# Performance work log

Hardware: AMD Instinct MI355X
Metric: run time of the kernel (lower is better)

The kernel has to match this reference:

```python
import jax, jax.numpy as jnp
import numpy as np

B, T, L = 64, 256, 64          # batch, time steps, num_links
H = 128                        # hidden_size
E = 524288                     # num edges
N = B * T                      # nodes seen by GCNConv
IN = L + L * L                 # 4160: concat of link features + flattened distance matrix
OUT = 12 * L                   # fc output size
NUM_LSTM = 2


def setup_inputs() -> dict:
    key = jax.random.key(0)
    ks = jax.random.split(key, 24)
    inp = {
        "x": jax.random.normal(ks[0], (B, T, L), jnp.float32),
        "distance": jax.random.uniform(ks[1], (L, L), jnp.float32),
        "edge_index": jax.random.randint(ks[2], (2, E), 0, N, jnp.int64),
    }
    # GCN layer params (PyG GCNConv: lin weight [in,out] acting as x @ W, bias after aggregation)
    dims = [IN, H, H, H]
    for i in range(3):
        s = 1.0 / np.sqrt(dims[i])
        inp[f"gcn_W{i}"] = jax.random.normal(ks[3 + 2 * i], (dims[i], H), jnp.float32) * s
        inp[f"gcn_b{i}"] = jnp.zeros((H,), jnp.float32)
    # LSTM params, torch layout: W_ih [4H, Hin], W_hh [4H, H], gate order i,f,g,o
    s = 1.0 / np.sqrt(H)
    for l in range(NUM_LSTM):
        inp[f"Wih{l}"] = jax.random.normal(ks[10 + 4 * l], (4 * H, H), jnp.float32) * s
        inp[f"Whh{l}"] = jax.random.normal(ks[11 + 4 * l], (4 * H, H), jnp.float32) * s
        inp[f"bih{l}"] = jax.random.normal(ks[12 + 4 * l], (4 * H,), jnp.float32) * s
        inp[f"bhh{l}"] = jax.random.normal(ks[13 + 4 * l], (4 * H,), jnp.float32) * s
    inp["fc_W"] = jax.random.normal(ks[20], (OUT, H), jnp.float32) * s
    inp["fc_b"] = jnp.zeros((OUT,), jnp.float32)
    return inp


def _gcn(x, W, b, src, dst):
    # GCNConv with add_self_loops=True: out = D^-1/2 (A+I) D^-1/2 (x W) + b
    h = x @ W
    deg = jnp.ones((N,), h.dtype).at[dst].add(1.0)  # in-degree + self loop
    dinv = jax.lax.rsqrt(deg)
    norm = dinv[src] * dinv[dst]                    # [E]
    agg = jnp.zeros_like(h).at[dst].add(h[src] * norm[:, None])
    agg = agg + h * (dinv * dinv)[:, None]          # self-loop term
    return agg + b


def _lstm_layer(xs, Wih, Whh, bih, bhh):
    # xs: [T, B, Hin]
    bias = bih + bhh

    def step(carry, xt):
        h, c = carry
        g = xt @ Wih.T + h @ Whh.T + bias
        i, f, gg, o = jnp.split(g, 4, axis=-1)
        c = jax.nn.sigmoid(f) * c + jax.nn.sigmoid(i) * jnp.tanh(gg)
        h = jax.nn.sigmoid(o) * jnp.tanh(c)
        return (h, c), h

    h0 = jnp.zeros((xs.shape[1], H), xs.dtype)
    _, ys = jax.lax.scan(step, (h0, h0), xs)
    return ys


def reference(x, distance, gcn_W0, gcn_b0, gcn_W1, gcn_b1, gcn_W2, gcn_b2,
              Wih0, Whh0, bih0, bhh0, Wih1, Whh1, bih1, bhh1, fc_W, fc_b,
              edge_index):
    src, dst = edge_index[0], edge_index[1]
    xf = x.reshape(N, L)
    dist_flat = jnp.broadcast_to(distance.reshape(1, L * L), (N, L * L))
    feat = jnp.concatenate([xf, dist_flat], axis=1)  # [N, IN]
    for W, b in ((gcn_W0, gcn_b0), (gcn_W1, gcn_b1), (gcn_W2, gcn_b2)):
        feat = jax.nn.relu(_gcn(feat, W, b, src, dst))
    seq = feat.reshape(B, T, H).transpose(1, 0, 2)   # [T, B, H]
    seq = _lstm_layer(seq, Wih0, Whh0, bih0, bhh0)
    seq = _lstm_layer(seq, Wih1, Whh1, bih1, bhh1)
    last = seq[-1]                                   # [B, H]
    out = last @ fc_W.T + fc_b                       # [B, OUT]
    return out.reshape(B, 12, L)
```

## Files before the change

kernel.cpp:

```cpp
#include <hip/hip_runtime.h>
#include <hip/hip_bf16.h>
#include <cstdint>
#include <cstddef>

#define NB 64
#define NT 256
#define NL 64
#define NH 128
#define NN 16384
#define NE 524288
#define NG 512
#define NOUT 768


__global__ __launch_bounds__(256) void k_transpose(const float* __restrict__ W,
                                                   float* __restrict__ Wt,
                                                   int K, int Nout) {
  int i = blockIdx.x * 256 + threadIdx.x;
  if (i < K * Nout) {
    int k = i / Nout, n = i % Nout;
    Wt[n * K + k] = W[i];
  }
}

__global__ __launch_bounds__(256) void k_dvec(const float* __restrict__ dist,
                                              const float* __restrict__ W0,
                                              float* __restrict__ dvec) {
  __shared__ float red[256];
  int j = blockIdx.x;
  int t = threadIdx.x;
  float acc = 0.f;
  for (int m = t; m < 4096; m += 256)
    acc += dist[m] * W0[(size_t)(64 + m) * 128 + j];
  red[t] = acc;
  __syncthreads();
  for (int off = 128; off > 0; off >>= 1) {
    if (t < off) red[t] += red[t + off];
    __syncthreads();
  }
  if (t == 0) dvec[j] = red[0];
}

__global__ __launch_bounds__(256) void k_count(const int* __restrict__ dst,
                                               int* __restrict__ counts) {
  int i = blockIdx.x * 256 + threadIdx.x;
  atomicAdd(&counts[dst[i]], 1);
}

__global__ __launch_bounds__(256) void k_dinv(const int* __restrict__ counts,
                                              float* __restrict__ dinv) {
  int n = blockIdx.x * 256 + threadIdx.x;
  dinv[n] = rsqrtf((float)counts[n] + 1.0f);
}

__global__ __launch_bounds__(1024) void k_scan(const int* __restrict__ counts,
                                               int* __restrict__ rowstart) {
  __shared__ int part[1024];
  int t = threadIdx.x;
  int base = t * 16;
  int local[16];
  int s = 0;
#pragma unroll
  for (int i = 0; i < 16; i++) { local[i] = s; s += counts[base + i]; }
  part[t] = s;
  __syncthreads();
  for (int off = 1; off < 1024; off <<= 1) {
    int v = (t >= off) ? part[t - off] : 0;
    __syncthreads();
    part[t] += v;
    __syncthreads();
  }
  int prefix = (t == 0) ? 0 : part[t - 1];
#pragma unroll
  for (int i = 0; i < 16; i++) rowstart[base + i] = prefix + local[i];
  if (t == 1023) rowstart[16384] = part[1023];
}

__global__ __launch_bounds__(256) void k_fill(const int* __restrict__ src,
                                              const int* __restrict__ dst,
                                              const int* __restrict__ rowstart,
                                              int* __restrict__ fill,
                                              const float* __restrict__ dinv,
                                              int* __restrict__ csr_src,
                                              float* __restrict__ csr_nrm) {
  int e = blockIdx.x * 256 + threadIdx.x;
  int sN = src[e], dN = dst[e];
  int pos = rowstart[dN] + atomicAdd(&fill[dN], 1);
  csr_src[pos] = sN;
  csr_nrm[pos] = dinv[sN] * dinv[dN];
}

template <int K, bool RELU, bool PERMC = false>
__global__ __launch_bounds__(256) void k_gemm_abt(const float* __restrict__ A,
                                                  const float* __restrict__ Bm,
                                                  const float* __restrict__ bias0,
                                                  const float* __restrict__ bias1,
                                                  float* __restrict__ C, int Nn) {
  __shared__ float As[64][K + 1];
  __shared__ float Bs[64][K + 1];
  const int tid = threadIdx.x;
  const int bm = blockIdx.x, bn = blockIdx.y;
  const int VPR = K / 4;
  for (int i = tid; i < 64 * VPR; i += 256) {
    int r = i / VPR, v = (i % VPR) * 4;
    float4 q = *(const float4*)(A + (size_t)(bm * 64 + r) * K + v);
    As[r][v] = q.x; As[r][v + 1] = q.y; As[r][v + 2] = q.z; As[r][v + 3] = q.w;
  }
  for (int i = tid; i < 64 * VPR; i += 256) {
    int r = i / VPR, v = (i % VPR) * 4;
    float4 q = *(const float4*)(Bm + (size_t)(bn * 64 + r) * K + v);
    Bs[r][v] = q.x; Bs[r][v + 1] = q.y; Bs[r][v + 2] = q.z; Bs[r][v + 3] = q.w;
  }
  __syncthreads();
  const int tr = (tid >> 4) << 2;
  const int tc = (tid & 15) << 2;
  float acc[4][4] = {};
#pragma unroll 4
  for (int k = 0; k < K; k++) {
    float a0 = As[tr + 0][k], a1 = As[tr + 1][k], a2 = As[tr + 2][k], a3 = As[tr + 3][k];
    float b0 = Bs[tc + 0][k], b1 = Bs[tc + 1][k], b2 = Bs[tc + 2][k], b3 = Bs[tc + 3][k];
    acc[0][0] += a0 * b0; acc[0][1] += a0 * b1; acc[0][2] += a0 * b2; acc[0][3] += a0 * b3;
    acc[1][0] += a1 * b0; acc[1][1] += a1 * b1; acc[1][2] += a1 * b2; acc[1][3] += a1 * b3;
    acc[2][0] += a2 * b0; acc[2][1] += a2 * b1; acc[2][2] += a2 * b2; acc[2][3] += a2 * b3;
    acc[3][0] += a3 * b0; acc[3][1] += a3 * b1; acc[3][2] += a3 * b2; acc[3][3] += a3 * b3;
  }
#pragma unroll
  for (int i2 = 0; i2 < 4; i2++) {
    int row = bm * 64 + tr + i2;
#pragma unroll
    for (int j2 = 0; j2 < 4; j2++) {
      int col = bn * 64 + tc + j2;
      float v = acc[i2][j2];
      if (bias0) v += bias0[col];
      if (bias1) v += bias1[col];
      if (RELU) v = fmaxf(v, 0.f);
      int colw = PERMC ? ((col & 127) * 4 + (col >> 7)) : col;
      C[(size_t)row * Nn + colw] = v;
    }
  }
}

__global__ __launch_bounds__(256) void k_agg(const float* __restrict__ h,
                                             const int* __restrict__ rowstart,
                                             const int* __restrict__ csr_src,
                                             const float* __restrict__ csr_nrm,
                                             const float* __restrict__ dinv,
                                             const float* __restrict__ bias,
                                             float* __restrict__ out) {
  int node = blockIdx.x * 4 + (threadIdx.x >> 6);
  int lane = threadIdx.x & 63;
  int s = rowstart[node], e = rowstart[node + 1];
  float a0 = 0.f, a1 = 0.f;
  for (int p = s; p < e; p++) {
    int src = csr_src[p];
    float w = csr_nrm[p];
    a0 += h[(size_t)src * 128 + lane] * w;
    a1 += h[(size_t)src * 128 + 64 + lane] * w;
  }
  float di = dinv[node];
  float sw = di * di;
  a0 += h[(size_t)node * 128 + lane] * sw + bias[lane];
  a1 += h[(size_t)node * 128 + 64 + lane] * sw + bias[64 + lane];
  out[(size_t)node * 128 + lane] = fmaxf(a0, 0.f);
  out[(size_t)node * 128 + 64 + lane] = fmaxf(a1, 0.f);
}


template <int CTRL>
__device__ __forceinline__ float dppadd(float x) {
  int r = __builtin_amdgcn_update_dpp(0, __float_as_int(x), CTRL, 0xF, 0xF, true);
  return x + __int_as_float(r);
}

__device__ __forceinline__ float sigf(float x) {
  return 1.f / (1.f + __expf(-x));
}
__device__ __forceinline__ float tanhf_fast(float x) {
  return 1.f - 2.f / (__expf(2.f * x) + 1.f);
}

template <bool LAST_ONLY>
__global__ __launch_bounds__(512, 2) void k_lstm2(const float* __restrict__ pre,
                                                  const float* __restrict__ Whh,
                                                  float* __restrict__ yout) {
  __shared__ float hbuf[2][128];
  const int tid = threadIdx.x;
  const int b = blockIdx.x;
  const int c4 = tid & 3;
  const int u = tid >> 2;

  int hidx[8];
#pragma unroll
  for (int j = 0; j < 8; j++) hidx[j] = c4 * 8 + (((u & 7) + 2 * c4 + j) & 7);

  float4 Wv[4][8];
#pragma unroll
  for (int g = 0; g < 4; g++)
#pragma unroll
    for (int j = 0; j < 8; j++)
      Wv[g][j] = *(const float4*)(Whh + (size_t)(g * 128 + u) * 128 + hidx[j] * 4);

  if (tid < 128) hbuf[0][tid] = 0.f;
  float cs = 0.f;
  const float* preb = pre + (size_t)b * 256 * 512 + tid;
  float pcur = preb[0];
  __syncthreads();

#define LSTM_STEP(CUR, NXT, T)                                                 \
  {                                                                            \
    int tn = (T) + 1; if (tn > 255) tn = 255;                                  \
    float pnext = preb[(size_t)tn * 512];                                      \
    const float4* hp = (const float4*)&hbuf[CUR][0];                           \
    float a0 = (c4 == 0) ? pcur : 0.f;                                         \
    float a1 = (c4 == 1) ? pcur : 0.f;                                         \
    float a2 = (c4 == 2) ? pcur : 0.f;                                         \
    float a3 = (c4 == 3) ? pcur : 0.f;                                         \
    _Pragma("unroll")                                                          \
    for (int j = 0; j < 8; j++) {                                              \
      float4 hv = hp[hidx[j]];                                                 \
      float4 w0 = Wv[0][j], w1 = Wv[1][j], w2 = Wv[2][j], w3 = Wv[3][j];       \
      a0 = fmaf(w0.x, hv.x, a0); a0 = fmaf(w0.y, hv.y, a0);                    \
      a0 = fmaf(w0.z, hv.z, a0); a0 = fmaf(w0.w, hv.w, a0);                    \
      a1 = fmaf(w1.x, hv.x, a1); a1 = fmaf(w1.y, hv.y, a1);                    \
      a1 = fmaf(w1.z, hv.z, a1); a1 = fmaf(w1.w, hv.w, a1);                    \
      a2 = fmaf(w2.x, hv.x, a2); a2 = fmaf(w2.y, hv.y, a2);                    \
      a2 = fmaf(w2.z, hv.z, a2); a2 = fmaf(w2.w, hv.w, a2);                    \
      a3 = fmaf(w3.x, hv.x, a3); a3 = fmaf(w3.y, hv.y, a3);                    \
      a3 = fmaf(w3.z, hv.z, a3); a3 = fmaf(w3.w, hv.w, a3);                    \
    }                                                                          \
    a0 = dppadd<0xB1>(a0); a0 = dppadd<0x4E>(a0);                              \
    a1 = dppadd<0xB1>(a1); a1 = dppadd<0x4E>(a1);                              \
    a2 = dppadd<0xB1>(a2); a2 = dppadd<0x4E>(a2);                              \
    a3 = dppadd<0xB1>(a3); a3 = dppadd<0x4E>(a3);                              \
    float si = sigf(a0), sf = sigf(a1), tg = tanhf_fast(a2), so = sigf(a3);    \
    cs = sf * cs + si * tg;                                                    \
    float hnew = so * tanhf_fast(cs);                                          \
    if (c4 == 0) hbuf[NXT][u] = hnew;                                          \
    if (!LAST_ONLY) {                                                          \
      if (c4 == 1) yout[((size_t)b * 256 + (T)) * 128 + u] = hnew;             \
    } else if ((T) == 255) {                                                   \
      if (c4 == 1) yout[(size_t)b * 128 + u] = hnew;                           \
    }                                                                          \
    pcur = pnext;                                                              \
    __syncthreads();                                                           \
  }

  for (int t = 0; t < 256; t += 2) {
    LSTM_STEP(0, 1, t);
    LSTM_STEP(1, 0, t + 1);
  }
#undef LSTM_STEP
}


extern "C" void kernel_launch(void* const* d_in, const int* in_sizes, int n_in,
                              void* d_out, int out_size, void* d_ws, size_t ws_size,
                              hipStream_t stream) {
  const float* x    = (const float*)d_in[0];
  const float* dist = (const float*)d_in[1];
  const int*   ei   = (const int*)d_in[2];
  const float* W0   = (const float*)d_in[3];
  const float* b0   = (const float*)d_in[4];
  const float* W1   = (const float*)d_in[5];
  const float* b1   = (const float*)d_in[6];
  const float* W2   = (const float*)d_in[7];
  const float* b2   = (const float*)d_in[8];
  const float* Wih0 = (const float*)d_in[9];
  const float* Whh0 = (const float*)d_in[10];
  const float* bih0 = (const float*)d_in[11];
  const float* bhh0 = (const float*)d_in[12];
  const float* Wih1 = (const float*)d_in[13];
  const float* Whh1 = (const float*)d_in[14];
  const float* bih1 = (const float*)d_in[15];
  const float* bhh1 = (const float*)d_in[16];
  const float* fcW  = (const float*)d_in[17];
  const float* fcb  = (const float*)d_in[18];
  float* out = (float*)d_out;

  char* ws = (char*)d_ws;
  size_t off = 0;
  auto alloc = [&](size_t bytes) -> void* {
    void* p = ws + off;
    off += (bytes + 255) & ~(size_t)255;
    return p;
  };
  float* bufA     = (float*)alloc((size_t)NN * 128 * 4);
  float* bufB     = (float*)alloc((size_t)NN * 128 * 4);
  float* pre      = (float*)alloc((size_t)NN * 512 * 4);
  int*   csr_src  = (int*)alloc((size_t)NE * 4);
  float* csr_nrm  = (float*)alloc((size_t)NE * 4);
  int*   counts   = (int*)alloc((size_t)NN * 4);
  int*   fillc    = (int*)alloc((size_t)NN * 4);
  int*   rowstart = (int*)alloc((size_t)(NN + 1) * 4);
  float* dinv     = (float*)alloc((size_t)NN * 4);
  float* dvec     = (float*)alloc(128 * 4);
  float* hlast    = (float*)alloc(64 * 128 * 4);
  float* wt0      = (float*)alloc(128 * 64 * 4);
  float* wt1      = (float*)alloc(128 * 128 * 4);
  float* wt2      = (float*)alloc(128 * 128 * 4);
  (void)ws_size; (void)in_sizes; (void)n_in; (void)out_size;

  const int* srcIdx = ei;
  const int* dstIdx = ei + NE;

  hipMemsetAsync(counts, 0, (size_t)NN * 4, stream);
  hipMemsetAsync(fillc, 0, (size_t)NN * 4, stream);

  k_transpose<<<(64 * 128 + 255) / 256, 256, 0, stream>>>(W0, wt0, 64, 128);
  k_transpose<<<(128 * 128 + 255) / 256, 256, 0, stream>>>(W1, wt1, 128, 128);
  k_transpose<<<(128 * 128 + 255) / 256, 256, 0, stream>>>(W2, wt2, 128, 128);
  k_dvec<<<128, 256, 0, stream>>>(dist, W0, dvec);

  k_count<<<NE / 256, 256, 0, stream>>>(dstIdx, counts);
  k_scan<<<1, 1024, 0, stream>>>(counts, rowstart);
  k_dinv<<<NN / 256, 256, 0, stream>>>(counts, dinv);
  k_fill<<<NE / 256, 256, 0, stream>>>(srcIdx, dstIdx, rowstart, fillc, dinv,
                                       csr_src, csr_nrm);

  dim3 gH(NN / 64, 128 / 64);
  k_gemm_abt<64, false><<<gH, 256, 0, stream>>>(x, wt0, dvec, nullptr, bufB, 128);
  k_agg<<<NN / 4, 256, 0, stream>>>(bufB, rowstart, csr_src, csr_nrm, dinv, b0, bufA);
  k_gemm_abt<128, false><<<gH, 256, 0, stream>>>(bufA, wt1, nullptr, nullptr, bufB, 128);
  k_agg<<<NN / 4, 256, 0, stream>>>(bufB, rowstart, csr_src, csr_nrm, dinv, b1, bufA);
  k_gemm_abt<128, false><<<gH, 256, 0, stream>>>(bufA, wt2, nullptr, nullptr, bufB, 128);
  k_agg<<<NN / 4, 256, 0, stream>>>(bufB, rowstart, csr_src, csr_nrm, dinv, b2, bufA);

  dim3 gP(NN / 64, 512 / 64);
  k_gemm_abt<128, false, true><<<gP, 256, 0, stream>>>(bufA, Wih0, bih0, bhh0, pre, 512);
  k_lstm2<false><<<64, 512, 0, stream>>>(pre, Whh0, bufB);
  k_gemm_abt<128, false, true><<<gP, 256, 0, stream>>>(bufB, Wih1, bih1, bhh1, pre, 512);
  k_lstm2<true><<<64, 512, 0, stream>>>(pre, Whh1, hlast);

  dim3 gF(1, NOUT / 64);
  k_gemm_abt<128, false><<<gF, 256, 0, stream>>>(hlast, fcW, fcb, nullptr, out, NOUT);
}
```

Measured before the change: 912.3 us.

## Split LSTM recurrence across 8 lanes per unit and pack CSR entries

The LSTM recurrence kernel now uses 1024 threads per batch row, with 8 lanes per hidden unit each holding a 16-wide slice of the recurrent weights. Partial sums are combined with DPP plus a ds_swizzle step, and the shared hidden buffer is padded so the vector reads avoid bank conflicts. This halves the serial FMA chain per step, at the cost of more reduction work and a larger block to synchronise. Separately, CSR source index and norm are packed into one int2, and the aggregation kernel reads float2 features with the edge loop unrolled by two, which cuts memory transactions in the gather.

```diff
diff --git a/kernel.cpp b/kernel.cpp
--- a/kernel.cpp
+++ b/kernel.cpp
@@ -81,13 +81,11 @@
                                               const int* __restrict__ rowstart,
                                               int* __restrict__ fill,
                                               const float* __restrict__ dinv,
-                                              int* __restrict__ csr_src,
-                                              float* __restrict__ csr_nrm) {
+                                              int2* __restrict__ csr) {
   int e = blockIdx.x * 256 + threadIdx.x;
   int sN = src[e], dN = dst[e];
   int pos = rowstart[dN] + atomicAdd(&fill[dN], 1);
-  csr_src[pos] = sN;
-  csr_nrm[pos] = dinv[sN] * dinv[dN];
+  csr[pos] = make_int2(sN, __float_as_int(dinv[sN] * dinv[dN]));
 }
 
 template <int K, bool RELU, bool PERMC = false>
@@ -142,27 +140,42 @@
 
 __global__ __launch_bounds__(256) void k_agg(const float* __restrict__ h,
                                              const int* __restrict__ rowstart,
-                                             const int* __restrict__ csr_src,
-                                             const float* __restrict__ csr_nrm,
+                                             const int2* __restrict__ csr,
                                              const float* __restrict__ dinv,
                                              const float* __restrict__ bias,
                                              float* __restrict__ out) {
   int node = blockIdx.x * 4 + (threadIdx.x >> 6);
   int lane = threadIdx.x & 63;
   int s = rowstart[node], e = rowstart[node + 1];
-  float a0 = 0.f, a1 = 0.f;
-  for (int p = s; p < e; p++) {
-    int src = csr_src[p];
-    float w = csr_nrm[p];
-    a0 += h[(size_t)src * 128 + lane] * w;
-    a1 += h[(size_t)src * 128 + 64 + lane] * w;
+  const float2* h2 = (const float2*)h;
+  float ax = 0.f, ay = 0.f;
+  int p = s;
+  for (; p + 1 < e; p += 2) {
+    int2 pk0 = csr[p];
+    int2 pk1 = csr[p + 1];
+    float2 hv0 = h2[(size_t)pk0.x * 64 + lane];
+    float2 hv1 = h2[(size_t)pk1.x * 64 + lane];
+    float w0 = __int_as_float(pk0.y);
+    float w1 = __int_as_float(pk1.y);
+    ax = fmaf(hv0.x, w0, ax); ay = fmaf(hv0.y, w0, ay);
+    ax = fmaf(hv1.x, w1, ax); ay = fmaf(hv1.y, w1, ay);
+  }
+  if (p < e) {
+    int2 pk0 = csr[p];
+    float2 hv0 = h2[(size_t)pk0.x * 64 + lane];
+    float w0 = __int_as_float(pk0.y);
+    ax = fmaf(hv0.x, w0, ax); ay = fmaf(hv0.y, w0, ay);
   }
   float di = dinv[node];
   float sw = di * di;
-  a0 += h[(size_t)node * 128 + lane] * sw + bias[lane];
-  a1 += h[(size_t)node * 128 + 64 + lane] * sw + bias[64 + lane];
-  out[(size_t)node * 128 + lane] = fmaxf(a0, 0.f);
-  out[(size_t)node * 128 + 64 + lane] = fmaxf(a1, 0.f);
+  float2 hs = h2[(size_t)node * 64 + lane];
+  float2 bv = ((const float2*)bias)[lane];
+  ax = fmaf(hs.x, sw, ax) + bv.x;
+  ay = fmaf(hs.y, sw, ay) + bv.y;
+  float2 o;
+  o.x = fmaxf(ax, 0.f);
+  o.y = fmaxf(ay, 0.f);
+  ((float2*)out)[(size_t)node * 64 + lane] = o;
 }
 
 
@@ -171,6 +184,10 @@
   int r = __builtin_amdgcn_update_dpp(0, __float_as_int(x), CTRL, 0xF, 0xF, true);
   return x + __int_as_float(r);
 }
+__device__ __forceinline__ float swzadd4(float x) {
+  int r = __builtin_amdgcn_ds_swizzle(__float_as_int(x), 0x101F);
+  return x + __int_as_float(r);
+}
 
 __device__ __forceinline__ float sigf(float x) {
   return 1.f / (1.f + __expf(-x));
@@ -179,73 +196,83 @@
   return 1.f - 2.f / (__expf(2.f * x) + 1.f);
 }
 
+typedef float f4v __attribute__((ext_vector_type(4)));
+
 template <bool LAST_ONLY>
-__global__ __launch_bounds__(512, 2) void k_lstm2(const float* __restrict__ pre,
-                                                  const float* __restrict__ Whh,
-                                                  float* __restrict__ yout) {
-  __shared__ float hbuf[2][128];
+__global__ __launch_bounds__(1024, 4) void k_lstm3(const float* __restrict__ pre,
+                                                   const float* __restrict__ Whh,
+                                                   float* __restrict__ yout) {
+  __shared__ float hbuf[2][160];
   const int tid = threadIdx.x;
   const int b = blockIdx.x;
-  const int c4 = tid & 3;
-  const int u = tid >> 2;
-
-  int hidx[8];
-#pragma unroll
-  for (int j = 0; j < 8; j++) hidx[j] = c4 * 8 + (((u & 7) + 2 * c4 + j) & 7);
-
-  float4 Wv[4][8];
+  const int e = tid & 7;
+  const int u = tid >> 3;
+
+  f4v Wv[4][4];
 #pragma unroll
   for (int g = 0; g < 4; g++)
 #pragma unroll
-    for (int j = 0; j < 8; j++)
-      Wv[g][j] = *(const float4*)(Whh + (size_t)(g * 128 + u) * 128 + hidx[j] * 4);
-
-  if (tid < 128) hbuf[0][tid] = 0.f;
+    for (int j = 0; j < 4; j++)
+      Wv[g][j] = *(const f4v*)(Whh + (size_t)(g * 128 + u) * 128 + e * 16 + j * 4);
+
+  if (tid < 160) hbuf[0][tid] = 0.f;
   float cs = 0.f;
-  const float* preb = pre + (size_t)b * 256 * 512 + tid;
+  const float* preb = pre + (size_t)b * NT * NG + (u * 4 + (e & 3));
   float pcur = preb[0];
+  const int rdoff = e * 20;
+  const int wroff = (u >> 4) * 20 + (u & 15);
+  float* ybase = LAST_ONLY ? (yout + (size_t)b * NH + u)
+                           : (yout + (size_t)b * NT * NH + u);
   __syncthreads();
 
 #define LSTM_STEP(CUR, NXT, T)                                                 \
   {                                                                            \
-    int tn = (T) + 1; if (tn > 255) tn = 255;                                  \
-    float pnext = preb[(size_t)tn * 512];                                      \
-    const float4* hp = (const float4*)&hbuf[CUR][0];                           \
-    float a0 = (c4 == 0) ? pcur : 0.f;                                         \
-    float a1 = (c4 == 1) ? pcur : 0.f;                                         \
-    float a2 = (c4 == 2) ? pcur : 0.f;                                         \
-    float a3 = (c4 == 3) ? pcur : 0.f;                                         \
-    _Pragma("unroll")                                                          \
-    for (int j = 0; j < 8; j++) {                                              \
-      float4 hv = hp[hidx[j]];                                                 \
-      float4 w0 = Wv[0][j], w1 = Wv[1][j], w2 = Wv[2][j], w3 = Wv[3][j];       \
-      a0 = fmaf(w0.x, hv.x, a0); a0 = fmaf(w0.y, hv.y, a0);                    \
-      a0 = fmaf(w0.z, hv.z, a0); a0 = fmaf(w0.w, hv.w, a0);                    \
-      a1 = fmaf(w1.x, hv.x, a1); a1 = fmaf(w1.y, hv.y, a1);                    \
-      a1 = fmaf(w1.z, hv.z, a1); a1 = fmaf(w1.w, hv.w, a1);                    \
-      a2 = fmaf(w2.x, hv.x, a2); a2 = fmaf(w2.y, hv.y, a2);                    \
-      a2 = fmaf(w2.z, hv.z, a2); a2 = fmaf(w2.w, hv.w, a2);                    \
-      a3 = fmaf(w3.x, hv.x, a3); a3 = fmaf(w3.y, hv.y, a3);                    \
-      a3 = fmaf(w3.z, hv.z, a3); a3 = fmaf(w3.w, hv.w, a3);                    \
-    }                                                                          \
-    a0 = dppadd<0xB1>(a0); a0 = dppadd<0x4E>(a0);                              \
-    a1 = dppadd<0xB1>(a1); a1 = dppadd<0x4E>(a1);                              \
-    a2 = dppadd<0xB1>(a2); a2 = dppadd<0x4E>(a2);                              \
-    a3 = dppadd<0xB1>(a3); a3 = dppadd<0x4E>(a3);                              \
-    float si = sigf(a0), sf = sigf(a1), tg = tanhf_fast(a2), so = sigf(a3);    \
+    int tn = (T) + 1; if (tn > NT - 1) tn = NT - 1;                            \
+    float pnext = preb[(size_t)tn * NG];                                       \
+    const float* hr = &hbuf[CUR][rdoff];                                       \
+    f4v h0 = *(const f4v*)(hr);                                                \
+    f4v h1 = *(const f4v*)(hr + 4);                                            \
+    f4v h2 = *(const f4v*)(hr + 8);                                            \
+    f4v h3 = *(const f4v*)(hr + 12);                                           \
+    f4v a0 = {0.f, 0.f, 0.f, 0.f}, a1 = a0, a2 = a0, a3 = a0;                  \
+    a0 = __builtin_elementwise_fma(Wv[0][0], h0, a0);                          \
+    a1 = __builtin_elementwise_fma(Wv[1][0], h0, a1);                          \
+    a2 = __builtin_elementwise_fma(Wv[2][0], h0, a2);                          \
+    a3 = __builtin_elementwise_fma(Wv[3][0], h0, a3);                          \
+    a0 = __builtin_elementwise_fma(Wv[0][1], h1, a0);                          \
+    a1 = __builtin_elementwise_fma(Wv[1][1], h1, a1);                          \
+    a2 = __builtin_elementwise_fma(Wv[2][1], h1, a2);                          \
+    a3 = __builtin_elementwise_fma(Wv[3][1], h1, a3);                          \
+    a0 = __builtin_elementwise_fma(Wv[0][2], h2, a0);                          \
+    a1 = __builtin_elementwise_fma(Wv[1][2], h2, a1);                          \
+    a2 = __builtin_elementwise_fma(Wv[2][2], h2, a2);                          \
+    a3 = __builtin_elementwise_fma(Wv[3][2], h2, a3);                          \
+    a0 = __builtin_elementwise_fma(Wv[0][3], h3, a0);                          \
+    a1 = __builtin_elementwise_fma(Wv[1][3], h3, a1);                          \
+    a2 = __builtin_elementwise_fma(Wv[2][3], h3, a2);                          \
+    a3 = __builtin_elementwise_fma(Wv[3][3], h3, a3);                          \
+    float s0 = (a0.x + a0.y) + (a0.z + a0.w) + ((e == 0) ? pcur : 0.f);        \
+    float s1 = (a1.x + a1.y) + (a1.z + a1.w) + ((e == 1) ? pcur : 0.f);        \
+    float s2 = (a2.x + a2.y) + (a2.z + a2.w) + ((e == 2) ? pcur : 0.f);        \
+    float s3 = (a3.x + a3.y) + (a3.z + a3.w) + ((e == 3) ? pcur : 0.f);        \
+    s0 = dppadd<0xB1>(s0); s0 = dppadd<0x4E>(s0); s0 = swzadd4(s0);            \
+    s1 = dppadd<0xB1>(s1); s1 = dppadd<0x4E>(s1); s1 = swzadd4(s1);            \
+    s2 = dppadd<0xB1>(s2); s2 = dppadd<0x4E>(s2); s2 = swzadd4(s2);            \
+    s3 = dppadd<0xB1>(s3); s3 = dppadd<0x4E>(s3); s3 = swzadd4(s3);            \
+    float si = sigf(s0), sf = sigf(s1), tg = tanhf_fast(s2), so = sigf(s3);    \
     cs = sf * cs + si * tg;                                                    \
     float hnew = so * tanhf_fast(cs);                                          \
-    if (c4 == 0) hbuf[NXT][u] = hnew;                                          \
+    if (e == 0) hbuf[NXT][wroff] = hnew;                                       \
     if (!LAST_ONLY) {                                                          \
-      if (c4 == 1) yout[((size_t)b * 256 + (T)) * 128 + u] = hnew;             \
-    } else if ((T) == 255) {                                                   \
-      if (c4 == 1) yout[(size_t)b * 128 + u] = hnew;                           \
+      if (e == 1) ybase[(size_t)(T) * NH] = hnew;                              \
+    } else if ((T) == NT - 1) {                                                \
+      if (e == 1) *ybase = hnew;                                               \
     }                                                                          \
     pcur = pnext;                                                              \
     __syncthreads();                                                           \
   }
 
-  for (int t = 0; t < 256; t += 2) {
+  for (int t = 0; t < NT; t += 2) {
     LSTM_STEP(0, 1, t);
     LSTM_STEP(1, 0, t + 1);
   }
@@ -287,8 +314,7 @@
   float* bufA     = (float*)alloc((size_t)NN * 128 * 4);
   float* bufB     = (float*)alloc((size_t)NN * 128 * 4);
   float* pre      = (float*)alloc((size_t)NN * 512 * 4);
-  int*   csr_src  = (int*)alloc((size_t)NE * 4);
-  float* csr_nrm  = (float*)alloc((size_t)NE * 4);
+  int2*  csr      = (int2*)alloc((size_t)NE * 8);
   int*   counts   = (int*)alloc((size_t)NN * 4);
   int*   fillc    = (int*)alloc((size_t)NN * 4);
   int*   rowstart = (int*)alloc((size_t)(NN + 1) * 4);
@@ -314,22 +340,21 @@
   k_count<<<NE / 256, 256, 0, stream>>>(dstIdx, counts);
   k_scan<<<1, 1024, 0, stream>>>(counts, rowstart);
   k_dinv<<<NN / 256, 256, 0, stream>>>(counts, dinv);
-  k_fill<<<NE / 256, 256, 0, stream>>>(srcIdx, dstIdx, rowstart, fillc, dinv,
-                                       csr_src, csr_nrm);
+  k_fill<<<NE / 256, 256, 0, stream>>>(srcIdx, dstIdx, rowstart, fillc, dinv, csr);
 
   dim3 gH(NN / 64, 128 / 64);
   k_gemm_abt<64, false><<<gH, 256, 0, stream>>>(x, wt0, dvec, nullptr, bufB, 128);
-  k_agg<<<NN / 4, 256, 0, stream>>>(bufB, rowstart, csr_src, csr_nrm, dinv, b0, bufA);
+  k_agg<<<NN / 4, 256, 0, stream>>>(bufB, rowstart, csr, dinv, b0, bufA);
   k_gemm_abt<128, false><<<gH, 256, 0, stream>>>(bufA, wt1, nullptr, nullptr, bufB, 128);
-  k_agg<<<NN / 4, 256, 0, stream>>>(bufB, rowstart, csr_src, csr_nrm, dinv, b1, bufA);
+  k_agg<<<NN / 4, 256, 0, stream>>>(bufB, rowstart, csr, dinv, b1, bufA);
   k_gemm_abt<128, false><<<gH, 256, 0, stream>>>(bufA, wt2, nullptr, nullptr, bufB, 128);
-  k_agg<<<NN / 4, 256, 0, stream>>>(bufB, rowstart, csr_src, csr_nrm, dinv, b2, bufA);
+  k_agg<<<NN / 4, 256, 0, stream>>>(bufB, rowstart, csr, dinv, b2, bufA);
 
   dim3 gP(NN / 64, 512 / 64);
   k_gemm_abt<128, false, true><<<gP, 256, 0, stream>>>(bufA, Wih0, bih0, bhh0, pre, 512);
-  k_lstm2<false><<<64, 512, 0, stream>>>(pre, Whh0, bufB);
+  k_lstm3<false><<<64, 1024, 0, stream>>>(pre, Whh0, bufB);
   k_gemm_abt<128, false, true><<<gP, 256, 0, stream>>>(bufB, Wih1, bih1, bhh1, pre, 512);
-  k_lstm2<true><<<64, 512, 0, stream>>>(pre, Whh1, hlast);
+  k_lstm3<true><<<64, 1024, 0, stream>>>(pre, Whh1, hlast);
 
   dim3 gF(1, NOUT / 64);
   k_gemm_abt<128, false><<<gF, 256, 0, stream>>>(hlast, fcW, fcb, nullptr, out, NOUT);
```

Result: slower. 1.107 ms (+21.3%).
